# Kernel optimization log

Measured on AMD Instinct MI355X. Metric: run time of the kernel, lower is better.

The kernel has to match this reference:

```python
import jax, jax.numpy as jnp
import numpy as np


def setup_inputs() -> dict:
    key = jax.random.key(0)
    k1, k2, k3, k4, k5 = jax.random.split(key, 5)
    B, C, V, D, O = 8, 64, 25000, 12, 64
    x = jax.random.normal(k1, (B, C, V), dtype=jnp.float32)
    nbr_idx = jax.random.randint(k2, (B, V, D), 0, V, dtype=jnp.int32)
    # true 1-ring valence in [1, D]
    deg = jax.random.randint(k3, (B, V), 1, D + 1, dtype=jnp.int32)
    # conv weight [O, C, 1, 2] flattened to [O, C, 2], fan-in init scale
    W = jax.random.normal(k4, (O, C, 2), dtype=jnp.float32) * (1.0 / np.sqrt(C * 2))
    b = jax.random.normal(k5, (O,), dtype=jnp.float32) * 0.01
    return {"x": x, "nbr_idx": nbr_idx, "deg": deg, "W": W, "b": b}


def reference(x, nbr_idx, deg, W, b):
    # x: [B, C, V]; nbr_idx: [B, V, D] padded 1-ring; deg: [B, V] valid count
    B, C, V = x.shape
    D = nbr_idx.shape[-1]
    # gather neighbor features: [B, C, V, D]
    gathered = jax.vmap(lambda xb, ib: xb[:, ib])(x, nbr_idx)
    mask = (jnp.arange(D, dtype=deg.dtype)[None, None, :] < deg[:, :, None])  # [B, V, D]
    maskf = mask.astype(x.dtype)[:, None, :, :]  # [B, 1, V, D]
    denom = jnp.maximum(deg, 1).astype(x.dtype)[:, None, :]  # [B, 1, V]
    nbr_mean = jnp.sum(gathered * maskf, axis=-1) / denom  # [B, C, V]
    # G: [B, C, V, 2] = (self feature, 1-ring mean); conv2d kernel (1,2)
    G = jnp.stack([x, nbr_mean], axis=-1)
    out = jnp.einsum('bcvk,ock->bov', G, W) + b[None, :, None]
    return out[..., None]  # [B, O, V, 1]
```

## Files before the change

kernel.cpp:

```cpp
#include <hip/hip_runtime.h>
#include <stdint.h>


#define NB 8
#define NC 64
#define NV 25000
#define ND 12
#define NO 64
#define VROW 32
#define ATL 391
#define NTB 782
#define GTB 256

typedef uint32_t u32x4 __attribute__((ext_vector_type(4)));
typedef uint32_t u32x2 __attribute__((ext_vector_type(2)));
typedef __bf16  bf16x8 __attribute__((ext_vector_type(8)));
typedef float   f32x4  __attribute__((ext_vector_type(4)));

__device__ inline uint32_t bf16pack(float a, float b) {
    uint32_t ua = __float_as_uint(a), ub = __float_as_uint(b);
    ua = (ua + 0x7fffu + ((ua >> 16) & 1u)) >> 16;
    ub = (ub + 0x7fffu + ((ub >> 16) & 1u)) >> 16;
    return ua | (ub << 16);
}
__device__ inline float blo(uint32_t u) { return __uint_as_float(u << 16); }
__device__ inline float bhi(uint32_t u) { return __uint_as_float(u & 0xffff0000u); }

__global__ __launch_bounds__(256) void wt_kernel(const float* __restrict__ W,
                                                 uint32_t* __restrict__ Wcb) {
    int i = blockIdx.x * 256 + threadIdx.x;
    int m = i >> 5;
    int c = (i & 31) * 2;
    int k = m >> 6;
    int o = m & 63;
    float s0 = W[o * (NC * 2) + c * 2 + k];
    float s1 = W[o * (NC * 2) + (c + 1) * 2 + k];
    Wcb[i] = bf16pack(s0, s1);
}

__global__ __launch_bounds__(512, 6) void ygemm5(const float* __restrict__ x,
                                                 const uint32_t* __restrict__ Wcb,
                                                 const float* __restrict__ bias,
                                                 uint32_t* __restrict__ y0,
                                                 uint32_t* __restrict__ y1) {
    __shared__ uint32_t lb[64 * 36];
    const int b = blockIdx.x & 7;
    const int tile = blockIdx.x >> 3;
    const int vbase = tile * 64;
    const int lane = threadIdx.x & 63, wave = threadIdx.x >> 6;
    const float* xb = x + (size_t)b * NC * NV;

    {
        int vg = vbase + lane;
        if (vg >= NV) vg = NV - 1;
#pragma unroll
        for (int pp = 0; pp < 4; ++pp) {
            const int p = wave * 4 + pp;
            const int c = p * 2;
            float s0 = __builtin_nontemporal_load(xb + (size_t)c * NV + vg);
            float s1 = __builtin_nontemporal_load(xb + (size_t)(c + 1) * NV + vg);
            lb[lane * 36 + p] = bf16pack(s0, s1);
        }
    }
    __syncthreads();

    const int l15 = lane & 15, lq = lane >> 4;
    const int pl  = wave >> 2;
    const int sub = wave & 3;

    union BF { u32x4 q; bf16x8 v; } bfr[2];
#pragma unroll
    for (int kt = 0; kt < 2; ++kt)
        bfr[kt].q = *reinterpret_cast<const u32x4*>(
            &lb[(sub * 16 + l15) * 36 + kt * 16 + lq * 4]);

    f32x4 acc[4];
#pragma unroll
    for (int mt = 0; mt < 4; ++mt) acc[mt] = (f32x4){0.f, 0.f, 0.f, 0.f};

#pragma unroll
    for (int kt = 0; kt < 2; ++kt) {
#pragma unroll
        for (int mt = 0; mt < 4; ++mt) {
            union { u32x4 q; bf16x8 v; } au;
            au.q = *(const u32x4*)(Wcb + (size_t)(pl * 64 + mt * 16 + l15) * 32
                                       + kt * 16 + lq * 4);
            acc[mt] = __builtin_amdgcn_mfma_f32_16x16x32_bf16(au.v, bfr[kt].v,
                                                              acc[mt], 0, 0, 0);
        }
    }

    const int v = vbase + sub * 16 + l15;
    if (v < NV) {
        if (pl == 0) {
            uint32_t* yr0 = y0 + ((size_t)b * NV + v) * VROW;
#pragma unroll
            for (int mt = 0; mt < 4; ++mt) {
                f32x4 a = acc[mt];
                const float* bp = bias + mt * 16 + lq * 4;
                a[0] += bp[0]; a[1] += bp[1]; a[2] += bp[2]; a[3] += bp[3];
                u32x2 p0 = {bf16pack(a[0], a[1]), bf16pack(a[2], a[3])};
                __builtin_nontemporal_store(p0, (u32x2*)(yr0 + mt * 8 + lq * 2));
            }
        } else {
            uint32_t* yr1 = y1 + ((size_t)b * NV + v) * VROW;
#pragma unroll
            for (int mt = 0; mt < 4; ++mt) {
                f32x4 a = acc[mt];
                u32x2 p1 = {bf16pack(a[0], a[1]), bf16pack(a[2], a[3])};
                *(u32x2*)(yr1 + mt * 8 + lq * 2) = p1;
            }
        }
    }
}

__global__ __launch_bounds__(256) void gather3(const int* __restrict__ nbr,
                                               const int* __restrict__ deg,
                                               const uint32_t* __restrict__ y0,
                                               const uint32_t* __restrict__ y1,
                                               float* __restrict__ out) {
    __shared__ float lds[2][32 * 68];

    const int b = blockIdx.x & 7;
    const int t0 = blockIdx.x >> 3;
    const int lane = threadIdx.x & 63;
    const int wave = threadIdx.x >> 6;
    const int s8 = lane >> 3;
    const int j = lane & 7;
    const int vloc = wave * 8 + s8;

    const int* nbrb = nbr + (size_t)b * NV * ND;
    const int* degb = deg + (size_t)b * NV;
    const uint32_t* y0b = y0 + (size_t)b * NV * VROW;
    const uint32_t* y1b = y1 + (size_t)b * NV * VROW;
    float* outb = out + (size_t)b * NO * NV;

    int idx[ND];
    int dg;
    u32x4 su;
    {
        int v = t0 * 32 + vloc;
        const int vc = v < NV ? v : NV - 1;
        const int4* p = reinterpret_cast<const int4*>(nbrb + (size_t)vc * ND);
        int4 a0 = p[0], a1 = p[1], a2 = p[2];
        idx[0] = a0.x; idx[1] = a0.y; idx[2]  = a0.z; idx[3]  = a0.w;
        idx[4] = a1.x; idx[5] = a1.y; idx[6]  = a1.z; idx[7]  = a1.w;
        idx[8] = a2.x; idx[9] = a2.y; idx[10] = a2.z; idx[11] = a2.w;
        dg = degb[vc];
        su = *(reinterpret_cast<const u32x4*>(y0b + (size_t)vc * VROW) + j);
    }

    int buf = 0;
    for (int t = t0; t < NTB; t += GTB) {
        u32x4 rows[ND];
#pragma unroll
        for (int d = 0; d < ND; ++d) {
            if (d < dg)
                rows[d] = *(reinterpret_cast<const u32x4*>(
                                y1b + (size_t)idx[d] * VROW) + j);
        }

        const int tn = (t + GTB < NTB) ? t + GTB : t;
        int idxn[ND];
        int dgn;
        u32x4 sun;
        {
            int v = tn * 32 + vloc;
            const int vc = v < NV ? v : NV - 1;
            const int4* p = reinterpret_cast<const int4*>(nbrb + (size_t)vc * ND);
            int4 a0 = p[0], a1 = p[1], a2 = p[2];
            idxn[0] = a0.x; idxn[1] = a0.y; idxn[2]  = a0.z; idxn[3]  = a0.w;
            idxn[4] = a1.x; idxn[5] = a1.y; idxn[6]  = a1.z; idxn[7]  = a1.w;
            idxn[8] = a2.x; idxn[9] = a2.y; idxn[10] = a2.z; idxn[11] = a2.w;
            dgn = degb[vc];
            sun = *(reinterpret_cast<const u32x4*>(y0b + (size_t)vc * VROW) + j);
        }

        const float inv = 1.0f / (float)dg;
        float ns[8];
#pragma unroll
        for (int k = 0; k < 8; ++k) ns[k] = 0.0f;
#pragma unroll
        for (int d = 0; d < ND; ++d) {
            if (d < dg) {
                u32x4 u = rows[d];
                ns[0] += blo(u[0]); ns[1] += bhi(u[0]);
                ns[2] += blo(u[1]); ns[3] += bhi(u[1]);
                ns[4] += blo(u[2]); ns[5] += bhi(u[2]);
                ns[6] += blo(u[3]); ns[7] += bhi(u[3]);
            }
        }

        {
            float f[8];
            f[0] = __builtin_fmaf(inv, ns[0], blo(su[0]));
            f[1] = __builtin_fmaf(inv, ns[1], bhi(su[0]));
            f[2] = __builtin_fmaf(inv, ns[2], blo(su[1]));
            f[3] = __builtin_fmaf(inv, ns[3], bhi(su[1]));
            f[4] = __builtin_fmaf(inv, ns[4], blo(su[2]));
            f[5] = __builtin_fmaf(inv, ns[5], bhi(su[2]));
            f[6] = __builtin_fmaf(inv, ns[6], blo(su[3]));
            f[7] = __builtin_fmaf(inv, ns[7], bhi(su[3]));
            f32x4 w0 = {f[0], f[1], f[2], f[3]};
            f32x4 w1 = {f[4], f[5], f[6], f[7]};
            *reinterpret_cast<f32x4*>(&lds[buf][vloc * 68 + j * 8])     = w0;
            *reinterpret_cast<f32x4*>(&lds[buf][vloc * 68 + j * 8 + 4]) = w1;
        }
        __syncthreads();

        {
            const int vl = threadIdx.x & 31;
            const int o8 = threadIdx.x >> 5;
            const int vv = t * 32 + vl;
            if (vv < NV) {
#pragma unroll
                for (int oo = 0; oo < 8; ++oo) {
                    const int o = oo * 8 + o8;
                    __builtin_nontemporal_store(lds[buf][vl * 68 + o],
                                                outb + (size_t)o * NV + vv);
                }
            }
        }

        buf ^= 1;
        dg = dgn;
        su = sun;
#pragma unroll
        for (int d = 0; d < ND; ++d) idx[d] = idxn[d];
    }
}

__global__ __launch_bounds__(64) void fallback_kernel(const float* __restrict__ x,
                                                      const int* __restrict__ nbr,
                                                      const int* __restrict__ deg,
                                                      const float* __restrict__ W,
                                                      const float* __restrict__ bias,
                                                      float* __restrict__ out) {
    const int bvi = blockIdx.x;
    const int b = bvi / NV, v = bvi % NV;
    const int o = threadIdx.x;
    const int degv = deg[bvi];
    const float inv = 1.0f / (float)degv;
    float acc = bias[o];
    for (int c = 0; c < NC; ++c) {
        const float* xc = x + ((size_t)b * NC + c) * NV;
        float m = 0.0f;
        for (int d = 0; d < degv; ++d) m += xc[nbr[(size_t)bvi * ND + d]];
        acc += W[o * (NC * 2) + c * 2] * xc[v] + W[o * (NC * 2) + c * 2 + 1] * (m * inv);
    }
    out[((size_t)b * NO + o) * NV + v] = acc;
}

extern "C" void kernel_launch(void* const* d_in, const int* in_sizes, int n_in,
                              void* d_out, int out_size, void* d_ws, size_t ws_size,
                              hipStream_t stream) {
    const float* x    = (const float*)d_in[0];
    const int*   nbr  = (const int*)d_in[1];
    const int*   deg  = (const int*)d_in[2];
    const float* W    = (const float*)d_in[3];
    const float* bias = (const float*)d_in[4];
    float* out = (float*)d_out;

    const size_t wcb_dw = 4096;
    const size_t plane  = (size_t)NB * NV * VROW;
    const size_t need = (wcb_dw + 2 * plane) * 4;
    if (ws_size >= need) {
        uint32_t* Wcb = (uint32_t*)d_ws;
        uint32_t* y0  = Wcb + wcb_dw;
        uint32_t* y1  = y0 + plane;
        wt_kernel<<<dim3(16), 256, 0, stream>>>(W, Wcb);
        ygemm5<<<dim3(NB * ATL), 512, 0, stream>>>(x, Wcb, bias, y0, y1);
        gather3<<<dim3(NB * GTB), 256, 0, stream>>>(nbr, deg, y0, y1, out);
    } else {
        fallback_kernel<<<dim3(NB * NV), 64, 0, stream>>>(x, nbr, deg, W, bias, out);
    }
}
```

Measured before the change: 184.0 us.

## Double GEMM vertex tile and stage outputs through swizzled LDS for coalesced stores

The projection GEMM kernel now handles 128 vertices per block instead of 64. It loads x with 8-byte vector loads and reuses each weight fragment across two MFMA B tiles. Results are written into XOR-swizzled shared memory and then copied out as fully coalesced 16-byte row stores to y0/y1, replacing scattered 8-byte per-lane global stores. The cost is more LDS per block, an extra barrier, and a lower occupancy hint (4 instead of 6).

```diff
diff --git a/kernel.cpp b/kernel.cpp
--- a/kernel.cpp
+++ b/kernel.cpp
@@ -8,7 +8,7 @@
 #define ND 12
 #define NO 64
 #define VROW 32
-#define ATL 391
+#define NGT 196
 #define NTB 782
 #define GTB 256
 
@@ -38,45 +38,63 @@
     Wcb[i] = bf16pack(s0, s1);
 }
 
-__global__ __launch_bounds__(512, 6) void ygemm5(const float* __restrict__ x,
+__global__ __launch_bounds__(512, 4) void ygemm6(const float* __restrict__ x,
                                                  const uint32_t* __restrict__ Wcb,
                                                  const float* __restrict__ bias,
                                                  uint32_t* __restrict__ y0,
                                                  uint32_t* __restrict__ y1) {
-    __shared__ uint32_t lb[64 * 36];
+    __shared__ uint32_t lb[4608 + 4096];
+    uint32_t* yst0 = lb;
+    uint32_t* yst1 = lb + 4608;
+
     const int b = blockIdx.x & 7;
     const int tile = blockIdx.x >> 3;
-    const int vbase = tile * 64;
-    const int lane = threadIdx.x & 63, wave = threadIdx.x >> 6;
+    const int vbase = tile * 128;
+    const int t = threadIdx.x;
+    const int lane = t & 63, wave = t >> 6;
     const float* xb = x + (size_t)b * NC * NV;
 
     {
-        int vg = vbase + lane;
-        if (vg >= NV) vg = NV - 1;
+        int vg = vbase + lane * 2;
+        if (vg > NV - 2) vg = NV - 2;
+        const int key = ((lane >> 1) & 7) << 2;
 #pragma unroll
         for (int pp = 0; pp < 4; ++pp) {
             const int p = wave * 4 + pp;
             const int c = p * 2;
-            float s0 = __builtin_nontemporal_load(xb + (size_t)c * NV + vg);
-            float s1 = __builtin_nontemporal_load(xb + (size_t)(c + 1) * NV + vg);
-            lb[lane * 36 + p] = bf16pack(s0, s1);
+            u32x2 qa = __builtin_nontemporal_load(
+                reinterpret_cast<const u32x2*>(xb + (size_t)c * NV + vg));
+            u32x2 qb = __builtin_nontemporal_load(
+                reinterpret_cast<const u32x2*>(xb + (size_t)(c + 1) * NV + vg));
+            const int pc = p ^ key;
+            lb[(lane * 2)     * 36 + pc] =
+                bf16pack(__uint_as_float(qa[0]), __uint_as_float(qb[0]));
+            lb[(lane * 2 + 1) * 36 + pc] =
+                bf16pack(__uint_as_float(qa[1]), __uint_as_float(qb[1]));
         }
     }
     __syncthreads();
 
     const int l15 = lane & 15, lq = lane >> 4;
-    const int pl  = wave >> 2;
-    const int sub = wave & 3;
-
-    union BF { u32x4 q; bf16x8 v; } bfr[2];
-#pragma unroll
-    for (int kt = 0; kt < 2; ++kt)
-        bfr[kt].q = *reinterpret_cast<const u32x4*>(
-            &lb[(sub * 16 + l15) * 36 + kt * 16 + lq * 4]);
-
-    f32x4 acc[4];
-#pragma unroll
-    for (int mt = 0; mt < 4; ++mt) acc[mt] = (f32x4){0.f, 0.f, 0.f, 0.f};
+    const int pl = wave >> 2, sub = wave & 3;
+
+    union BF { u32x4 q; bf16x8 v; } bfr[2][2];
+#pragma unroll
+    for (int s = 0; s < 2; ++s) {
+        const int vl = sub * 32 + s * 16 + l15;
+        const int key = ((vl >> 2) & 7) << 2;
+#pragma unroll
+        for (int kt = 0; kt < 2; ++kt)
+            bfr[s][kt].q = *reinterpret_cast<const u32x4*>(
+                &lb[vl * 36 + ((kt * 16 + lq * 4) ^ key)]);
+    }
+    __syncthreads();
+
+    f32x4 acc[2][4];
+#pragma unroll
+    for (int s = 0; s < 2; ++s)
+#pragma unroll
+        for (int mt = 0; mt < 4; ++mt) acc[s][mt] = (f32x4){0.f, 0.f, 0.f, 0.f};
 
 #pragma unroll
     for (int kt = 0; kt < 2; ++kt) {
@@ -85,30 +103,44 @@
             union { u32x4 q; bf16x8 v; } au;
             au.q = *(const u32x4*)(Wcb + (size_t)(pl * 64 + mt * 16 + l15) * 32
                                        + kt * 16 + lq * 4);
-            acc[mt] = __builtin_amdgcn_mfma_f32_16x16x32_bf16(au.v, bfr[kt].v,
-                                                              acc[mt], 0, 0, 0);
-        }
-    }
-
-    const int v = vbase + sub * 16 + l15;
-    if (v < NV) {
-        if (pl == 0) {
-            uint32_t* yr0 = y0 + ((size_t)b * NV + v) * VROW;
-#pragma unroll
-            for (int mt = 0; mt < 4; ++mt) {
-                f32x4 a = acc[mt];
+#pragma unroll
+            for (int s = 0; s < 2; ++s)
+                acc[s][mt] = __builtin_amdgcn_mfma_f32_16x16x32_bf16(au.v, bfr[s][kt].v,
+                                                                     acc[s][mt], 0, 0, 0);
+        }
+    }
+
+    uint32_t* yst = pl ? yst1 : yst0;
+#pragma unroll
+    for (int s = 0; s < 2; ++s) {
+        const int vrow = sub * 32 + s * 16 + l15;
+        const int key = (vrow & 7) << 2;
+#pragma unroll
+        for (int mt = 0; mt < 4; ++mt) {
+            f32x4 a = acc[s][mt];
+            if (pl == 0) {
                 const float* bp = bias + mt * 16 + lq * 4;
                 a[0] += bp[0]; a[1] += bp[1]; a[2] += bp[2]; a[3] += bp[3];
-                u32x2 p0 = {bf16pack(a[0], a[1]), bf16pack(a[2], a[3])};
-                __builtin_nontemporal_store(p0, (u32x2*)(yr0 + mt * 8 + lq * 2));
             }
-        } else {
-            uint32_t* yr1 = y1 + ((size_t)b * NV + v) * VROW;
-#pragma unroll
-            for (int mt = 0; mt < 4; ++mt) {
-                f32x4 a = acc[mt];
-                u32x2 p1 = {bf16pack(a[0], a[1]), bf16pack(a[2], a[3])};
-                *(u32x2*)(yr1 + mt * 8 + lq * 2) = p1;
+            u32x2 pk = {bf16pack(a[0], a[1]), bf16pack(a[2], a[3])};
+            *reinterpret_cast<u32x2*>(&yst[vrow * 32 + ((mt * 8 + lq * 2) ^ key)]) = pk;
+        }
+    }
+    __syncthreads();
+
+    {
+        uint32_t* y0g = y0 + ((size_t)b * NV + vbase) * VROW;
+        uint32_t* y1g = y1 + ((size_t)b * NV + vbase) * VROW;
+#pragma unroll
+        for (int h = 0; h < 2; ++h) {
+            const int ck = t + h * 512;
+            const int r = ck >> 3;
+            if (vbase + r < NV) {
+                const int off = ((ck & 7) * 4) ^ ((r & 7) << 2);
+                u32x4 q0 = *reinterpret_cast<const u32x4*>(&yst0[r * 32 + off]);
+                __builtin_nontemporal_store(q0, reinterpret_cast<u32x4*>(y0g + ck * 4));
+                u32x4 q1 = *reinterpret_cast<const u32x4*>(&yst1[r * 32 + off]);
+                *reinterpret_cast<u32x4*>(y1g + ck * 4) = q1;
             }
         }
     }
@@ -269,7 +301,7 @@
         uint32_t* y0  = Wcb + wcb_dw;
         uint32_t* y1  = y0 + plane;
         wt_kernel<<<dim3(16), 256, 0, stream>>>(W, Wcb);
-        ygemm5<<<dim3(NB * ATL), 512, 0, stream>>>(x, Wcb, bias, y0, y1);
+        ygemm6<<<dim3(NB * NGT), 512, 0, stream>>>(x, Wcb, bias, y0, y1);
         gather3<<<dim3(NB * GTB), 256, 0, stream>>>(nbr, deg, y0, y1, out);
     } else {
         fallback_kernel<<<dim3(NB * NV), 64, 0, stream>>>(x, nbr, deg, W, bias, out);
```

Result: faster. 168.6 us (-8.4%).
